# Kernel tuning notes

Measured on AMD Instinct MI355X. Metric: run time of the kernel, lower is better.

Reference implementation:

```python
import jax, jax.numpy as jnp
import numpy as np

E = 8        # num_expert
D = 768      # d_model
H = 3072     # expert hidden = 4*d_model
K = 2        # top_k
N = 4096     # tokens
C = 2048


def setup_inputs() -> dict:
    key = jax.random.key(0)
    k0, k1, k2, k3 = jax.random.split(key, 4)
    moe_inp = jax.random.normal(k0, (N, D), dtype=jnp.float32)
    gate_w = jax.random.normal(k1, (D, E), dtype=jnp.float32) / np.sqrt(D).astype(np.float32)
    gate_b = jnp.zeros((E,), dtype=jnp.float32)
    w1 = jax.random.normal(k2, (E, D, H), dtype=jnp.float32) / np.sqrt(D).astype(np.float32)
    b1 = jnp.zeros((E, H), dtype=jnp.float32)
    w2 = jax.random.normal(k3, (E, H, D), dtype=jnp.float32) / np.sqrt(H).astype(np.float32)
    b2 = jnp.zeros((E, D), dtype=jnp.float32)
    return {"moe_inp": moe_inp, "gate_w": gate_w, "gate_b": gate_b,
            "w1": w1, "b1": b1, "w2": w2, "b2": b2}


def reference(moe_inp, gate_w, gate_b, w1, b1, w2, b2):
    # --- NaiveGate: linear scores, top-k experts, softmax over the k scores ---
    logits = moe_inp @ gate_w + gate_b                      # [N, E]
    top_v, top_i = jax.lax.top_k(logits, K)                 # [N, K]
    gate_score = jax.nn.softmax(top_v, axis=-1)             # [N, K]

    # --- scatter tokens to expert-contiguous capacity buffers (MOEScatter) ---
    flat_e = top_i.reshape(-1)                              # [N*K] expert id per slot
    onehot = jax.nn.one_hot(flat_e, E, dtype=jnp.int32)     # [N*K, E]
    # running position of each token inside its expert's buffer
    pos = jnp.sum(jnp.cumsum(onehot, axis=0) * onehot, axis=1) - 1  # [N*K]
    x_rep = jnp.repeat(moe_inp, K, axis=0)                  # [N*K, D]
    xe = jnp.zeros((E, C, D), dtype=moe_inp.dtype).at[flat_e, pos].set(x_rep, mode='drop')

    # --- grouped expert FFN (expert_fn): per-expert batched GEMMs ---
    h = jax.nn.gelu(jnp.einsum('ecd,edh->ech', xe, w1) + b1[:, None, :])
    ye = jnp.einsum('ech,ehd->ecd', h, w2) + b2[:, None, :]  # [E, C, D]

    # --- gather back to token order (MOEGather) and combine with gate scores ---
    y_flat = ye.at[flat_e, pos].get(mode='fill', fill_value=0.0)  # [N*K, D]
    out = jnp.einsum('nkd,nk->nd', y_flat.reshape(N, K, D), gate_score)
    return out
```

## Files before the change

kernel.cpp:

```cpp
#include <hip/hip_runtime.h>
#include <hip/hip_bf16.h>
#include <math.h>

#define NT    4096
#define DM    768
#define HD    3072
#define NE    8
#define CAP   2048
#define SLOTS_MAX 9216

typedef __attribute__((ext_vector_type(8))) short bf16x8;
typedef __attribute__((ext_vector_type(4))) float f32x4;

__device__ __forceinline__ unsigned short f2bf(float f) {
  unsigned int u = __float_as_uint(f);
  unsigned int r = (u + 0x7fffu + ((u >> 16) & 1u)) >> 16;
  return (unsigned short)r;
}

__device__ __forceinline__ void async16(const unsigned short* g, unsigned short* l) {
  __builtin_amdgcn_global_load_lds((const __attribute__((address_space(1))) void*)g,
                                   (__attribute__((address_space(3))) void*)l,
                                   16, 0, 0);
}

__global__ void convert_x_kernel(const float* __restrict__ x,
                                 unsigned short* __restrict__ xb) {
  int i = (blockIdx.x * 256 + threadIdx.x) * 4;
  float4 v = *(const float4*)(x + i);
  uint2 o;
  o.x = (unsigned int)f2bf(v.x) | ((unsigned int)f2bf(v.y) << 16);
  o.y = (unsigned int)f2bf(v.z) | ((unsigned int)f2bf(v.w) << 16);
  *(uint2*)(xb + i) = o;
}

__global__ void transpose_kernel(const float* __restrict__ src,
                                 unsigned short* __restrict__ dst,
                                 int R, int src_stride, int col_off,
                                 size_t src_e_stride, size_t dst_e_stride) {
  __shared__ unsigned short tile[64][34];
  const float* s = src + blockIdx.z * src_e_stride;
  unsigned short* d = dst + blockIdx.z * dst_e_stride;
  const int r0 = blockIdx.y * 32;
  const int c0 = blockIdx.x * 64;
  const int t = threadIdx.x;
#pragma unroll
  for (int i = 0; i < 4; i++) {
    int row = (t >> 5) + i * 8;
    int cu  = t & 31;
    const float2 v = *(const float2*)(s + (size_t)(r0 + row) * src_stride + col_off + c0 + cu * 2);
    tile[cu * 2][row]     = f2bf(v.x);
    tile[cu * 2 + 1][row] = f2bf(v.y);
  }
  __syncthreads();
#pragma unroll
  for (int i = 0; i < 4; i++) {
    int drow = (t >> 4) + i * 16;
    int ru   = t & 15;
    unsigned int v = *(const unsigned int*)&tile[drow][ru * 2];
    *(unsigned int*)(d + (size_t)(c0 + drow) * R + r0 + ru * 2) = v;
  }
}

__global__ void gate_dots_kernel(const float* __restrict__ inp,
                                 const float* __restrict__ gw,
                                 const float* __restrict__ gb,
                                 int2* __restrict__ tope,
                                 float2* __restrict__ tops) {
  const int tok  = blockIdx.x * 4 + (threadIdx.x >> 6);
  const int lane = threadIdx.x & 63;
  const float* x = inp + (size_t)tok * DM;
  float acc[NE];
#pragma unroll
  for (int e = 0; e < NE; e++) acc[e] = 0.f;
  for (int d = lane; d < DM; d += 64) {
    float xv = x[d];
    const float4 w0 = *(const float4*)(gw + d * NE);
    const float4 w1v = *(const float4*)(gw + d * NE + 4);
    acc[0] += xv * w0.x; acc[1] += xv * w0.y;
    acc[2] += xv * w0.z; acc[3] += xv * w0.w;
    acc[4] += xv * w1v.x; acc[5] += xv * w1v.y;
    acc[6] += xv * w1v.z; acc[7] += xv * w1v.w;
  }
#pragma unroll
  for (int e = 0; e < NE; e++) {
    float v = acc[e];
#pragma unroll
    for (int m = 32; m > 0; m >>= 1) v += __shfl_xor(v, m, 64);
    acc[e] = v + gb[e];
  }
  if (lane == 0) {
    float bv = -1e30f, sv = -1e30f; int bi = 0, si = 0;
#pragma unroll
    for (int e = 0; e < NE; e++) {
      float v = acc[e];
      if (v > bv)      { sv = bv; si = bi; bv = v; bi = e; }
      else if (v > sv) { sv = v;  si = e; }
    }
    float e1 = expf(sv - bv);
    float s0 = 1.f / (1.f + e1);
    float s1 = e1 / (1.f + e1);
    tope[tok] = make_int2(bi, si);
    tops[tok] = make_float2(s0, s1);
  }
}

__device__ __forceinline__ int agg_inc(int* lcnt, int key) {
  const int lane = threadIdx.x & 63;
  int p = 0;
#pragma unroll
  for (int ee = 0; ee < NE; ee++) {
    unsigned long long m = __ballot(key == ee);
    if (m) {
      int leader = __ffsll(m) - 1;
      int n = __popcll(m);
      int b = 0;
      if (lane == leader) b = atomicAdd(&lcnt[ee], n);
      b = __shfl(b, leader, 64);
      if (key == ee) p = b + __popcll(m & ((1ull << lane) - 1ull));
    }
  }
  return p;
}

__global__ void assign_kernel(const int2* __restrict__ tope,
                              int* __restrict__ cnt,
                              int* __restrict__ base,
                              int* __restrict__ src,
                              int2* __restrict__ pos) {
  __shared__ int lcnt[NE];
  const int t = threadIdx.x;
  if (t < NE) lcnt[t] = 0;
  __syncthreads();
  for (int i = t; i < NT; i += 1024) {
    int2 e = tope[i];
    int p0 = agg_inc(lcnt, e.x);
    int p1 = agg_inc(lcnt, e.y);
    if (p0 < CAP) src[e.x * CAP + p0] = i;
    if (p1 < CAP) src[e.y * CAP + p1] = i;
    pos[i] = make_int2(p0, p1);
  }
  __syncthreads();
  if (t == 0) {
    int b = 0;
    for (int e = 0; e < NE; e++) {
      int c = min(lcnt[e], CAP);
      cnt[e] = c;
      base[e] = b;
      b += (c + 127) & ~127;
    }
  }
}

__global__ __launch_bounds__(256) void gemm1_kernel(
    const unsigned short* __restrict__ xb,
    const unsigned short* __restrict__ w1t,
    const float* __restrict__ b1,
    const int* __restrict__ cnt,
    const int* __restrict__ base,
    const int* __restrict__ src,
    unsigned short* __restrict__ h,
    int hoff, int chunk) {
  const int b = blockIdx.x;
  const int e = b & 7;
  const int idx = b >> 3;
  const int m0 = (idx & 15) * 128;
  const int n0 = (idx >> 4) * 128;
  const int count = cnt[e];
  if (m0 >= count) return;
  const int hb = base[e];

  __shared__ unsigned short As[2][128 * 32];
  __shared__ unsigned short Bs[2][128 * 32];

  const int t = threadIdx.x;
  const int lane = t & 63;
  const int wave = t >> 6;
  const int r0 = t >> 2;
  const int kc = (t & 3) * 8;

  const int tok0 = (m0 + r0      < count) ? src[e * CAP + m0 + r0]      : 0;
  const int tok1 = (m0 + r0 + 64 < count) ? src[e * CAP + m0 + r0 + 64] : 0;
  const unsigned short* aptr0 = xb + (size_t)tok0 * DM + kc;
  const unsigned short* aptr1 = xb + (size_t)tok1 * DM + kc;
  const unsigned short* w1e = w1t + (size_t)e * chunk * DM;
  const unsigned short* bptr0 = w1e + (size_t)(n0 + r0) * DM + kc;
  const unsigned short* bptr1 = bptr0 + (size_t)64 * DM;

  const int wrow = (wave >> 1) * 64;
  const int wcol = (wave & 1) * 64;
  const int lrow = lane & 15;
  const int koff = (lane >> 4) * 8;

  f32x4 acc[4][4];
#pragma unroll
  for (int i = 0; i < 4; i++)
#pragma unroll
    for (int j = 0; j < 4; j++) acc[i][j] = (f32x4){0.f, 0.f, 0.f, 0.f};

#define STAGE1(bi, kk) do {                                   \
    unsigned short* A_ = As[bi] + wave * 512;                 \
    unsigned short* B_ = Bs[bi] + wave * 512;                 \
    async16(aptr0 + (kk), A_);                                \
    async16(aptr1 + (kk), A_ + 2048);                         \
    async16(bptr0 + (kk), B_);                                \
    async16(bptr1 + (kk), B_ + 2048);                         \
  } while (0)

#define COMPUTE1(bi) do {                                               \
    const unsigned short* A_ = As[bi];                                  \
    const unsigned short* B_ = Bs[bi];                                  \
    bf16x8 af[4], bfr[4];                                               \
    _Pragma("unroll")                                                   \
    for (int i = 0; i < 4; i++)                                         \
      af[i] = *(const bf16x8*)(A_ + (wrow + i * 16 + lrow) * 32 + koff);\
    _Pragma("unroll")                                                   \
    for (int j = 0; j < 4; j++)                                         \
      bfr[j] = *(const bf16x8*)(B_ + (wcol + j * 16 + lrow) * 32 + koff);\
    _Pragma("unroll")                                                   \
    for (int i = 0; i < 4; i++)                                         \
      _Pragma("unroll")                                                 \
      for (int j = 0; j < 4; j++)                                       \
        acc[i][j] = __builtin_amdgcn_mfma_f32_16x16x32_bf16(af[i], bfr[j], acc[i][j], 0, 0, 0); \
  } while (0)

  const int NS = DM / 32;
  STAGE1(0, 0);
  __syncthreads();
  int buf = 0;
  for (int ts = 0; ts < NS - 1; ++ts) {
    STAGE1(buf ^ 1, (ts + 1) * 32);
    COMPUTE1(buf);
    __syncthreads();
    buf ^= 1;
  }
  COMPUTE1(buf);

  const int q4 = (lane >> 4) * 4;
  const int c = lane & 15;
  unsigned short* hrow = h + (size_t)(hb + m0) * chunk + n0;
#pragma unroll
  for (int j = 0; j < 4; j++) {
    const float bias = b1[e * HD + hoff + n0 + wcol + j * 16 + c];
#pragma unroll
    for (int i = 0; i < 4; i++) {
#pragma unroll
      for (int r = 0; r < 4; r++) {
        int m = wrow + i * 16 + q4 + r;
        float v = acc[i][j][r] + bias;
        float u2 = 1.5957691216f * (v + 0.044715f * v * v * v);
        float g = v / (1.f + __expf(-u2));
        hrow[(size_t)m * chunk + wcol + j * 16 + c] = f2bf(g);
      }
    }
  }
#undef STAGE1
#undef COMPUTE1
}

__global__ __launch_bounds__(256) void gemm2_kernel(
    const unsigned short* __restrict__ h,
    const unsigned short* __restrict__ w2t,
    const int* __restrict__ cnt,
    const int* __restrict__ base,
    float* __restrict__ ye,
    int chunk, int add_prev) {
  const int b = blockIdx.x;
  const int e = b & 7;
  const int kh = (b >> 3) & 1;
  const int idx = b >> 4;
  const int m0 = (idx & 15) * 128;
  const int n0 = (idx >> 4) * 128;
  const int count = cnt[e];
  if (m0 >= count) return;
  const int hb = base[e];
  const int khalf = chunk >> 1;

  __shared__ unsigned short As[2][128 * 32];
  __shared__ unsigned short Bs[2][128 * 32];

  const int t = threadIdx.x;
  const int lane = t & 63;
  const int wave = t >> 6;
  const int r0 = t >> 2;
  const int kc = (t & 3) * 8;

  const unsigned short* aptr0 = h + (size_t)(hb + m0 + r0) * chunk + kh * khalf + kc;
  const unsigned short* aptr1 = aptr0 + (size_t)64 * chunk;
  const unsigned short* w2e = w2t + (size_t)e * DM * chunk;
  const unsigned short* bptr0 = w2e + (size_t)(n0 + r0) * chunk + kh * khalf + kc;
  const unsigned short* bptr1 = bptr0 + (size_t)64 * chunk;

  const int wrow = (wave >> 1) * 64;
  const int wcol = (wave & 1) * 64;
  const int lrow = lane & 15;
  const int koff = (lane >> 4) * 8;

  f32x4 acc[4][4];
#pragma unroll
  for (int i = 0; i < 4; i++)
#pragma unroll
    for (int j = 0; j < 4; j++) acc[i][j] = (f32x4){0.f, 0.f, 0.f, 0.f};

#define STAGE2(bi, kk) do {                                   \
    unsigned short* A_ = As[bi] + wave * 512;                 \
    unsigned short* B_ = Bs[bi] + wave * 512;                 \
    async16(aptr0 + (kk), A_);                                \
    async16(aptr1 + (kk), A_ + 2048);                         \
    async16(bptr0 + (kk), B_);                                \
    async16(bptr1 + (kk), B_ + 2048);                         \
  } while (0)

#define COMPUTE2(bi) do {                                               \
    const unsigned short* A_ = As[bi];                                  \
    const unsigned short* B_ = Bs[bi];                                  \
    bf16x8 af[4], bfr[4];                                               \
    _Pragma("unroll")                                                   \
    for (int i = 0; i < 4; i++)                                         \
      af[i] = *(const bf16x8*)(A_ + (wrow + i * 16 + lrow) * 32 + koff);\
    _Pragma("unroll")                                                   \
    for (int j = 0; j < 4; j++)                                         \
      bfr[j] = *(const bf16x8*)(B_ + (wcol + j * 16 + lrow) * 32 + koff);\
    _Pragma("unroll")                                                   \
    for (int i = 0; i < 4; i++)                                         \
      _Pragma("unroll")                                                 \
      for (int j = 0; j < 4; j++)                                       \
        acc[i][j] = __builtin_amdgcn_mfma_f32_16x16x32_bf16(af[i], bfr[j], acc[i][j], 0, 0, 0); \
  } while (0)

  const int NS = khalf >> 5;
  STAGE2(0, 0);
  __syncthreads();
  int buf = 0;
  for (int ts = 0; ts < NS - 1; ++ts) {
    STAGE2(buf ^ 1, (ts + 1) * 32);
    COMPUTE2(buf);
    __syncthreads();
    buf ^= 1;
  }
  COMPUTE2(buf);

  const int q4 = (lane >> 4) * 4;
  const int c = lane & 15;
  float* yrow = ye + (size_t)kh * SLOTS_MAX * DM + (size_t)(hb + m0) * DM + n0;
#pragma unroll
  for (int i = 0; i < 4; i++) {
#pragma unroll
    for (int r = 0; r < 4; r++) {
      int m = wrow + i * 16 + q4 + r;
#pragma unroll
      for (int j = 0; j < 4; j++) {
        int n = wcol + j * 16 + c;
        float v = acc[i][j][r];
        if (add_prev) v += yrow[(size_t)m * DM + n];
        yrow[(size_t)m * DM + n] = v;
      }
    }
  }
#undef STAGE2
#undef COMPUTE2
}

__global__ void gather_kernel(const float* __restrict__ ye,
                              const float* __restrict__ b2,
                              const int2* __restrict__ tope,
                              const float2* __restrict__ tops,
                              const int2* __restrict__ pos,
                              const int* __restrict__ base,
                              float* __restrict__ out) {
  int idx = blockIdx.x * 256 + threadIdx.x;
  int tok = idx / (DM / 4);
  int d4 = (idx % (DM / 4)) * 4;
  int2 e = tope[tok];
  float2 s = tops[tok];
  int2 p = pos[tok];
  const float* ye1 = ye + (size_t)SLOTS_MAX * DM;
  float4 r = make_float4(0.f, 0.f, 0.f, 0.f);
  if (p.x < CAP) {
    size_t row = (size_t)(base[e.x] + p.x) * DM + d4;
    const float4 va = *(const float4*)(ye + row);
    const float4 vb = *(const float4*)(ye1 + row);
    const float4 bb = *(const float4*)(b2 + e.x * DM + d4);
    r.x += s.x * (va.x + vb.x + bb.x); r.y += s.x * (va.y + vb.y + bb.y);
    r.z += s.x * (va.z + vb.z + bb.z); r.w += s.x * (va.w + vb.w + bb.w);
  }
  if (p.y < CAP) {
    size_t row = (size_t)(base[e.y] + p.y) * DM + d4;
    const float4 va = *(const float4*)(ye + row);
    const float4 vb = *(const float4*)(ye1 + row);
    const float4 bb = *(const float4*)(b2 + e.y * DM + d4);
    r.x += s.y * (va.x + vb.x + bb.x); r.y += s.y * (va.y + vb.y + bb.y);
    r.z += s.y * (va.z + vb.z + bb.z); r.w += s.y * (va.w + vb.w + bb.w);
  }
  *(float4*)(out + (size_t)tok * DM + d4) = r;
}

extern "C" void kernel_launch(void* const* d_in, const int* in_sizes, int n_in,
                              void* d_out, int out_size, void* d_ws, size_t ws_size,
                              hipStream_t stream) {
  const float* inp = (const float*)d_in[0];
  const float* gw  = (const float*)d_in[1];
  const float* gb  = (const float*)d_in[2];
  const float* w1  = (const float*)d_in[3];
  const float* b1  = (const float*)d_in[4];
  const float* w2  = (const float*)d_in[5];
  const float* b2  = (const float*)d_in[6];
  float* out = (float*)d_out;

  const size_t meta = 164352;
  const int cands[8] = {3072, 1536, 1024, 768, 512, 384, 256, 128};
  int chunk = 128;
  for (int ci = 0; ci < 8; ci++) {
    int c = cands[ci];
    size_t need = meta + (size_t)NT * DM * 2
                + (size_t)NE * c * DM * 2
                + (size_t)SLOTS_MAX * c * 2
                + 2 * (size_t)SLOTS_MAX * DM * 4;
    if (need <= ws_size) { chunk = c; break; }
  }

  char* ws = (char*)d_ws;
  int*    cnt  = (int*)(ws);
  int*    base = (int*)(ws + 256);
  int*    srcb = (int*)(ws + 512);
  int2*   tope = (int2*)(ws + 66048);
  float2* tops = (float2*)(ws + 98816);
  int2*   pos  = (int2*)(ws + 131584);
  size_t off = meta;
  unsigned short* xb = (unsigned short*)(ws + off);  off += (size_t)NT * DM * 2;
  unsigned short* wt = (unsigned short*)(ws + off);  off += (size_t)NE * chunk * DM * 2;
  unsigned short* hc = (unsigned short*)(ws + off);  off += (size_t)SLOTS_MAX * chunk * 2;
  float* ye = (float*)(ws + off);

  convert_x_kernel<<<(NT * DM) / 1024, 256, 0, stream>>>(inp, xb);
  gate_dots_kernel<<<NT / 4, 256, 0, stream>>>(inp, gw, gb, tope, tops);
  assign_kernel<<<1, 1024, 0, stream>>>(tope, cnt, base, srcb, pos);

  for (int c = 0; c < HD; c += chunk) {
    transpose_kernel<<<dim3(chunk / 64, DM / 32, NE), 256, 0, stream>>>(
        w1, wt, DM, HD, c, (size_t)DM * HD, (size_t)chunk * DM);
    gemm1_kernel<<<NE * 16 * (chunk / 128), 256, 0, stream>>>(
        xb, wt, b1, cnt, base, srcb, hc, c, chunk);
    transpose_kernel<<<dim3(DM / 64, chunk / 32, NE), 256, 0, stream>>>(
        w2 + (size_t)c * DM, wt, chunk, DM, 0, (size_t)HD * DM, (size_t)DM * chunk);
    gemm2_kernel<<<NE * 2 * 16 * (DM / 128), 256, 0, stream>>>(
        hc, wt, cnt, base, ye, chunk, c == 0 ? 0 : 1);
  }

  gather_kernel<<<(NT * DM / 4) / 256, 256, 0, stream>>>(ye, b2, tope, tops, pos, base, out);
}
```

Baseline: 377.2 us.

## Triple-buffer GEMM LDS pipeline with XOR swizzle and expert-interleaved block order

Both expert GEMM kernels move from a double-buffered LDS pipeline to a triple-buffered one. Two K-tiles are kept in flight, with explicit vmcnt waits and raw s_barrier in place of __syncthreads. LDS columns are XOR-swizzled on both the async-load and fragment-read sides to cut bank conflicts. Block-index decoding is changed so n varies fastest and experts interleave, which improves reuse of the A/B tiles in L2. The transpose kernel also switches to a 1D grid with experts interleaved. In exchange, LDS use rises (occupancy may drop), and correctness depends on the hand-written waitcnt counts matching the four async loads per stage.

```diff
diff --git a/kernel.cpp b/kernel.cpp
--- a/kernel.cpp
+++ b/kernel.cpp
@@ -37,12 +37,18 @@
 __global__ void transpose_kernel(const float* __restrict__ src,
                                  unsigned short* __restrict__ dst,
                                  int R, int src_stride, int col_off,
-                                 size_t src_e_stride, size_t dst_e_stride) {
+                                 size_t src_e_stride, size_t dst_e_stride,
+                                 int nx) {
   __shared__ unsigned short tile[64][34];
-  const float* s = src + blockIdx.z * src_e_stride;
-  unsigned short* d = dst + blockIdx.z * dst_e_stride;
-  const int r0 = blockIdx.y * 32;
-  const int c0 = blockIdx.x * 64;
+  const int b = blockIdx.x;
+  const int e = b & 7;
+  const int idx = b >> 3;
+  const int bx = idx % nx;
+  const int by = idx / nx;
+  const float* s = src + (size_t)e * src_e_stride;
+  unsigned short* d = dst + (size_t)e * dst_e_stride;
+  const int r0 = by * 32;
+  const int c0 = bx * 64;
   const int t = threadIdx.x;
 #pragma unroll
   for (int i = 0; i < 4; i++) {
@@ -164,20 +170,21 @@
   const int b = blockIdx.x;
   const int e = b & 7;
   const int idx = b >> 3;
-  const int m0 = (idx & 15) * 128;
-  const int n0 = (idx >> 4) * 128;
+  const int nch = chunk >> 7;
+  const int n0 = (idx % nch) * 128;
+  const int m0 = (idx / nch) * 128;
   const int count = cnt[e];
   if (m0 >= count) return;
   const int hb = base[e];
 
-  __shared__ unsigned short As[2][128 * 32];
-  __shared__ unsigned short Bs[2][128 * 32];
+  __shared__ unsigned short As[3 * 4096];
+  __shared__ unsigned short Bs[3 * 4096];
 
   const int t = threadIdx.x;
   const int lane = t & 63;
   const int wave = t >> 6;
   const int r0 = t >> 2;
-  const int kc = (t & 3) * 8;
+  const int kc = ((t & 3) ^ ((t >> 3) & 3)) * 8;
 
   const int tok0 = (m0 + r0      < count) ? src[e * CAP + m0 + r0]      : 0;
   const int tok1 = (m0 + r0 + 64 < count) ? src[e * CAP + m0 + r0 + 64] : 0;
@@ -190,7 +197,7 @@
   const int wrow = (wave >> 1) * 64;
   const int wcol = (wave & 1) * 64;
   const int lrow = lane & 15;
-  const int koff = (lane >> 4) * 8;
+  const int koff = ((lane >> 4) ^ ((lane >> 1) & 3)) * 8;
 
   f32x4 acc[4][4];
 #pragma unroll
@@ -199,8 +206,8 @@
     for (int j = 0; j < 4; j++) acc[i][j] = (f32x4){0.f, 0.f, 0.f, 0.f};
 
 #define STAGE1(bi, kk) do {                                   \
-    unsigned short* A_ = As[bi] + wave * 512;                 \
-    unsigned short* B_ = Bs[bi] + wave * 512;                 \
+    unsigned short* A_ = As + (bi) * 4096 + wave * 512;       \
+    unsigned short* B_ = Bs + (bi) * 4096 + wave * 512;       \
     async16(aptr0 + (kk), A_);                                \
     async16(aptr1 + (kk), A_ + 2048);                         \
     async16(bptr0 + (kk), B_);                                \
@@ -208,8 +215,8 @@
   } while (0)
 
 #define COMPUTE1(bi) do {                                               \
-    const unsigned short* A_ = As[bi];                                  \
-    const unsigned short* B_ = Bs[bi];                                  \
+    const unsigned short* A_ = As + (bi) * 4096;                        \
+    const unsigned short* B_ = Bs + (bi) * 4096;                        \
     bf16x8 af[4], bfr[4];                                               \
     _Pragma("unroll")                                                   \
     for (int i = 0; i < 4; i++)                                         \
@@ -226,15 +233,25 @@
 
   const int NS = DM / 32;
   STAGE1(0, 0);
-  __syncthreads();
-  int buf = 0;
-  for (int ts = 0; ts < NS - 1; ++ts) {
-    STAGE1(buf ^ 1, (ts + 1) * 32);
-    COMPUTE1(buf);
-    __syncthreads();
-    buf ^= 1;
-  }
-  COMPUTE1(buf);
+  STAGE1(1, 32);
+  int cur = 0;
+  for (int ts = 0; ts < NS - 2; ++ts) {
+    int pf = cur + 2; if (pf >= 3) pf -= 3;
+    STAGE1(pf, (ts + 2) * 32);
+    asm volatile("s_waitcnt vmcnt(8)" ::: "memory");
+    __builtin_amdgcn_s_barrier();
+    COMPUTE1(cur);
+    asm volatile("s_waitcnt lgkmcnt(0)" ::: "memory");
+    __builtin_amdgcn_s_barrier();
+    if (++cur == 3) cur = 0;
+  }
+  asm volatile("s_waitcnt vmcnt(4)" ::: "memory");
+  __builtin_amdgcn_s_barrier();
+  COMPUTE1(cur);
+  if (++cur == 3) cur = 0;
+  asm volatile("s_waitcnt vmcnt(0)" ::: "memory");
+  __builtin_amdgcn_s_barrier();
+  COMPUTE1(cur);
 
   const int q4 = (lane >> 4) * 4;
   const int c = lane & 15;
@@ -267,23 +284,24 @@
     int chunk, int add_prev) {
   const int b = blockIdx.x;
   const int e = b & 7;
-  const int kh = (b >> 3) & 1;
-  const int idx = b >> 4;
-  const int m0 = (idx & 15) * 128;
-  const int n0 = (idx >> 4) * 128;
+  const int idx = b >> 3;
+  const int fast = idx % 12;
+  const int m0 = (idx / 12) * 128;
+  const int n0 = (fast >> 1) * 128;
+  const int kh = fast & 1;
   const int count = cnt[e];
   if (m0 >= count) return;
   const int hb = base[e];
   const int khalf = chunk >> 1;
 
-  __shared__ unsigned short As[2][128 * 32];
-  __shared__ unsigned short Bs[2][128 * 32];
+  __shared__ unsigned short As[3 * 4096];
+  __shared__ unsigned short Bs[3 * 4096];
 
   const int t = threadIdx.x;
   const int lane = t & 63;
   const int wave = t >> 6;
   const int r0 = t >> 2;
-  const int kc = (t & 3) * 8;
+  const int kc = ((t & 3) ^ ((t >> 3) & 3)) * 8;
 
   const unsigned short* aptr0 = h + (size_t)(hb + m0 + r0) * chunk + kh * khalf + kc;
   const unsigned short* aptr1 = aptr0 + (size_t)64 * chunk;
@@ -294,7 +312,7 @@
   const int wrow = (wave >> 1) * 64;
   const int wcol = (wave & 1) * 64;
   const int lrow = lane & 15;
-  const int koff = (lane >> 4) * 8;
+  const int koff = ((lane >> 4) ^ ((lane >> 1) & 3)) * 8;
 
   f32x4 acc[4][4];
 #pragma unroll
@@ -303,8 +321,8 @@
     for (int j = 0; j < 4; j++) acc[i][j] = (f32x4){0.f, 0.f, 0.f, 0.f};
 
 #define STAGE2(bi, kk) do {                                   \
-    unsigned short* A_ = As[bi] + wave * 512;                 \
-    unsigned short* B_ = Bs[bi] + wave * 512;                 \
+    unsigned short* A_ = As + (bi) * 4096 + wave * 512;       \
+    unsigned short* B_ = Bs + (bi) * 4096 + wave * 512;       \
     async16(aptr0 + (kk), A_);                                \
     async16(aptr1 + (kk), A_ + 2048);                         \
     async16(bptr0 + (kk), B_);                                \
@@ -312,8 +330,8 @@
   } while (0)
 
 #define COMPUTE2(bi) do {                                               \
-    const unsigned short* A_ = As[bi];                                  \
-    const unsigned short* B_ = Bs[bi];                                  \
+    const unsigned short* A_ = As + (bi) * 4096;                        \
+    const unsigned short* B_ = Bs + (bi) * 4096;                        \
     bf16x8 af[4], bfr[4];                                               \
     _Pragma("unroll")                                                   \
     for (int i = 0; i < 4; i++)                                         \
@@ -330,15 +348,25 @@
 
   const int NS = khalf >> 5;
   STAGE2(0, 0);
-  __syncthreads();
-  int buf = 0;
-  for (int ts = 0; ts < NS - 1; ++ts) {
-    STAGE2(buf ^ 1, (ts + 1) * 32);
-    COMPUTE2(buf);
-    __syncthreads();
-    buf ^= 1;
-  }
-  COMPUTE2(buf);
+  STAGE2(1, 32);
+  int cur = 0;
+  for (int ts = 0; ts < NS - 2; ++ts) {
+    int pf = cur + 2; if (pf >= 3) pf -= 3;
+    STAGE2(pf, (ts + 2) * 32);
+    asm volatile("s_waitcnt vmcnt(8)" ::: "memory");
+    __builtin_amdgcn_s_barrier();
+    COMPUTE2(cur);
+    asm volatile("s_waitcnt lgkmcnt(0)" ::: "memory");
+    __builtin_amdgcn_s_barrier();
+    if (++cur == 3) cur = 0;
+  }
+  asm volatile("s_waitcnt vmcnt(4)" ::: "memory");
+  __builtin_amdgcn_s_barrier();
+  COMPUTE2(cur);
+  if (++cur == 3) cur = 0;
+  asm volatile("s_waitcnt vmcnt(0)" ::: "memory");
+  __builtin_amdgcn_s_barrier();
+  COMPUTE2(cur);
 
   const int q4 = (lane >> 4) * 4;
   const int c = lane & 15;
@@ -437,12 +465,12 @@
   assign_kernel<<<1, 1024, 0, stream>>>(tope, cnt, base, srcb, pos);
 
   for (int c = 0; c < HD; c += chunk) {
-    transpose_kernel<<<dim3(chunk / 64, DM / 32, NE), 256, 0, stream>>>(
-        w1, wt, DM, HD, c, (size_t)DM * HD, (size_t)chunk * DM);
+    transpose_kernel<<<NE * (chunk / 64) * (DM / 32), 256, 0, stream>>>(
+        w1, wt, DM, HD, c, (size_t)DM * HD, (size_t)chunk * DM, chunk / 64);
     gemm1_kernel<<<NE * 16 * (chunk / 128), 256, 0, stream>>>(
         xb, wt, b1, cnt, base, srcb, hc, c, chunk);
-    transpose_kernel<<<dim3(DM / 64, chunk / 32, NE), 256, 0, stream>>>(
-        w2 + (size_t)c * DM, wt, chunk, DM, 0, (size_t)HD * DM, (size_t)DM * chunk);
+    transpose_kernel<<<NE * (DM / 64) * (chunk / 32), 256, 0, stream>>>(
+        w2 + (size_t)c * DM, wt, chunk, DM, 0, (size_t)HD * DM, (size_t)DM * chunk, DM / 64);
     gemm2_kernel<<<NE * 2 * 16 * (DM / 128), 256, 0, stream>>>(
         hc, wt, cnt, base, ye, chunk, c == 0 ? 0 : 1);
   }
```

Result: slower. 387.6 us (+2.7%).
